# Kernel optimization log

Hardware: AMD Instinct MI355X
Metric: run time of the kernel (lower is better)

## Reference

```python
import jax, jax.numpy as jnp
import numpy as np

E = 16          # num_experts
D_FULL = 1024   # full_feature_dim
DM = 128        # expert_dim
S = D_FULL // E # per-expert feature slice = 64
P = 2048        # num patches
B = 8
C = 256
W = 3           # local_window (neighbor experts)
DEPTH = 8       # cantor_depth
NEG = -1e9


def _cantor_coord(pos, max_len, depth):
    x = pos / max(1, max_len - 1)
    x = max(1e-6, min(x, 1.0 - 1e-6))
    val, factor = 0.0, 0.5
    for _ in range(depth):
        x *= 3.0
        d = int(x)
        x -= d
        if d == 2:
            val += factor
        factor *= 0.5
    return val


def _expert_routes():
    coords = np.array([_cantor_coord(i, E, DEPTH) for i in range(E)], dtype=np.float32)
    return np.stack([np.argsort(np.abs(coords - coords[i]), kind='stable')[:W] for i in range(E)]).astype(np.int32)


ROUTES = _expert_routes()  # [E, W] static routing table


def setup_inputs():
    key = jax.random.key(0)
    ks = jax.random.split(key, 8)
    h = S // 4
    lim = float(np.sqrt(6.0 / (S + DM)))  # xavier_uniform bound
    penta = jax.random.normal(ks[5], (E, 5, DM), jnp.float32) * 0.02
    penta = penta / jnp.linalg.norm(penta, axis=-1, keepdims=True)
    return {
        'tokens': jax.random.normal(ks[0], (B, P, D_FULL), jnp.float32),
        'fingerprints': jax.random.uniform(ks[1], (P,), jnp.float32),
        'alpha': jnp.ones((E,), jnp.float32),
        'gate_w1': jax.random.normal(ks[2], (E, S, h), jnp.float32) * 0.05,
        'gate_b1': jnp.zeros((E, h), jnp.float32),
        'gate_w2': jax.random.normal(ks[3], (E, h, 1), jnp.float32) * 0.05,
        'gate_b2': jnp.zeros((E, 1), jnp.float32),
        'q_w': jax.random.uniform(ks[4], (E, S, DM), jnp.float32, -lim, lim),
        'k_w': jax.random.uniform(ks[6], (E, S, DM), jnp.float32, -lim, lim),
        'v_w': jax.random.uniform(ks[7], (E, S, DM), jnp.float32, -lim, lim),
        'penta': penta,
        'fusion_w': jnp.ones((5,), jnp.float32) / 5.0,
        'temperature': jnp.float32(0.5),
    }


def _dispatch(fingerprints):
    # Fingerprint band masks, then fixed-capacity gather (static shapes for jit).
    masks = []
    for e in range(E):
        lo, hi = e / E, (e + 1) / E
        m = (fingerprints >= lo) & ((fingerprints <= hi) if e == E - 1 else (fingerprints < hi))
        masks.append(m)
    masks = jnp.stack(masks)                             # [E, P]
    order = jnp.argsort(jnp.where(masks, 0, 1), axis=1)  # stable: assigned patches first
    idx = order[:, :C]                                   # [E, C]
    valid = jnp.take_along_axis(masks, idx, axis=1)      # [E, C]
    return idx, valid


def _forward(tokens, fingerprints, alpha, gate_w1, gate_b1, gate_w2, gate_b2,
             q_w, k_w, v_w, penta, fusion_w, temperature):
    idx, valid = _dispatch(fingerprints)
    Kaff, Qaff, Vs = [], [], []
    for e in range(E):  # fixed structural loop over experts
        feats = tokens[:, idx[e], e * S:(e + 1) * S]                       # [B, C, S]
        g = jax.nn.sigmoid(jax.nn.gelu(feats @ gate_w1[e] + gate_b1[e]) @ gate_w2[e] + gate_b2[e])
        aw = jax.nn.sigmoid(alpha[e])
        feats = feats * (g * aw + (1.0 - aw))                              # gated features
        Q = feats @ q_w[e]
        K = feats @ k_w[e]
        V = feats @ v_w[e]                                                 # [B, C, DM]
        dirs = penta[e] / jnp.linalg.norm(penta[e], axis=-1, keepdims=True)  # [5, DM]
        Kaff.append(jnp.einsum('bcd,vd->vbc', K, dirs))
        Qaff.append(jnp.einsum('bcd,vd->vbc', Q, dirs))
        Vs.append(V)
    Kaff = jnp.stack(Kaff)   # [E, 5, B, C]
    Qaff = jnp.stack(Qaff)   # [E, 5, B, C]
    Vs = jnp.stack(Vs)       # [E, B, C, DM]
    wdir = jax.nn.softmax(fusion_w)
    vmask = valid.astype(jnp.float32)
    out = jnp.zeros((B, P, DM), jnp.float32)
    for e in range(E):
        nb = ROUTES[e]                                  # static [W]
        Knb, Vnb, vnb = Kaff[nb], Vs[nb], vmask[nb]     # [W,5,B,C], [W,B,C,DM], [W,C]
        scores = jnp.einsum('vbi,nvbj->vbinj', Qaff[e], Knb) / temperature
        scores = jnp.where(vnb[None, None, None, :, :] > 0, scores, NEG)
        attn = jax.nn.softmax(scores.reshape(5, B, C, W * C), axis=-1).reshape(5, B, C, W, C)
        att = jnp.einsum('vbinj,nbjd->vbid', attn, Vnb)  # per-direction attended values
        out_e = jnp.einsum('v,vbid->bid', wdir, att) * vmask[e][None, :, None]
        out = out.at[:, idx[e]].add(out_e)              # scatter back to patch positions
    return out


def reference(tokens, fingerprints, alpha, gate_w1, gate_b1, gate_w2, gate_b2,
              q_w, k_w, v_w, penta, fusion_w, temperature):
    return _forward(tokens, fingerprints, alpha, gate_w1, gate_b1, gate_w2, gate_b2,
                    q_w, k_w, v_w, penta, fusion_w, temperature)
```

## Files before the change

kernel.cpp:

```cpp
#include <hip/hip_runtime.h>
#include <cfloat>
#include <math.h>

#define E 16
#define DFULL 1024
#define DM 128
#define S 64
#define P 2048
#define B 8
#define C 256
#define W 3
#define H 16
#define RQ 16
#define NCH 16
#define RQ2 32
#define NCH2 8
#define LOG2E 1.4426950408889634f
#define WST 272

typedef __attribute__((ext_vector_type(8))) short short8;
typedef __attribute__((ext_vector_type(4))) float f32x4;
#define MFMA_BF16(a, b, c) __builtin_amdgcn_mfma_f32_16x16x32_bf16((a), (b), (c), 0, 0, 0)

#if defined(__HIP_DEVICE_COMPILE__) && __has_builtin(__builtin_amdgcn_exp2f)
#define EXP2(x) __builtin_amdgcn_exp2f(x)
#else
#define EXP2(x) exp2f(x)
#endif

struct RoutesArg { int nb[E][W]; };

static void compute_routes(int r[E][W]) {
  float coords[E];
  for (int i = 0; i < E; ++i) {
    double x = (double)i / (double)(E - 1);
    if (x < 1e-06) x = 1e-06;
    if (x > 1.0 - 1e-06) x = 1.0 - 1e-06;
    double val = 0.0, factor = 0.5;
    for (int k = 0; k < 8; ++k) {
      x *= 3.0;
      int d = (int)x;
      x -= (double)d;
      if (d == 2) val += factor;
      factor *= 0.5;
    }
    coords[i] = (float)val;
  }
  for (int e = 0; e < E; ++e) {
    float de[E];
    for (int i = 0; i < E; ++i) de[i] = fabsf(coords[i] - coords[e]);
    bool used[E] = {false};
    for (int w = 0; w < W; ++w) {
      int best = -1; float bd = FLT_MAX;
      for (int i = 0; i < E; ++i)
        if (!used[i] && de[i] < bd) { bd = de[i]; best = i; }
      used[best] = true;
      r[e][w] = best;
    }
  }
}

__device__ __forceinline__ unsigned short bfhi(float x) {
  return (unsigned short)(__float_as_uint(x) >> 16);
}
__device__ __forceinline__ float bf2f(unsigned short h) {
  return __uint_as_float(((unsigned)h) << 16);
}
__device__ __forceinline__ float gelu_tanh(float x) {
  float u = 0.7978845608028654f * (x + 0.044715f * x * x * x);
  float ez = __expf(2.0f * u);
  float th = 1.0f - __fdividef(2.0f, ez + 1.0f);
  return 0.5f * x * (1.0f + th);
}
__device__ __forceinline__ float sigmoidf_(float x) {
  return __fdividef(1.0f, 1.0f + __expf(-x));
}

__global__ __launch_bounds__(256) void k_setup(
    const float* __restrict__ fp, const float* __restrict__ qw,
    const float* __restrict__ kw, const float* __restrict__ penta,
    const float* __restrict__ temp, const float* __restrict__ vw,
    int* __restrict__ idx, int* __restrict__ counts,
    unsigned short* __restrict__ qkdT_h, unsigned short* __restrict__ qkdT_l,
    unsigned short* __restrict__ vwT_h, unsigned short* __restrict__ vwT_l) {
  int e = blockIdx.x, t = threadIdx.x;
  __shared__ float s_tr[DM * 65];
  if (blockIdx.y == 1) {
    const float* vwe = vw + (size_t)e * S * DM;
    for (int u = t; u < S * DM; u += 256) {
      int s = u >> 7, d = u & 127;
      s_tr[d * 65 + s] = vwe[u];
    }
    __syncthreads();
    for (int u = t; u < S * DM; u += 256) {
      int d = u >> 6, s = u & 63;
      float f = s_tr[d * 65 + s];
      unsigned short h = bfhi(f), l = bfhi(f - bf2f(h));
      vwT_h[(size_t)e * 8192 + u] = h;
      vwT_l[(size_t)e * 8192 + u] = l;
    }
    return;
  }
  {
    float lo = (float)e * 0.0625f, hi = (float)(e + 1) * 0.0625f;
    bool last = (e == E - 1);
    int p0 = t * 8;
    int m[8]; int ls = 0;
    #pragma unroll
    for (int k = 0; k < 8; ++k) {
      float f = fp[p0 + k];
      bool mm = (f >= lo) && (last ? (f <= hi) : (f < hi));
      m[k] = mm ? 1 : 0;
      ls += m[k];
    }
    __shared__ int sc[256];
    sc[t] = ls;
    __syncthreads();
    for (int o = 1; o < 256; o <<= 1) {
      int v = (t >= o) ? sc[t - o] : 0;
      __syncthreads();
      sc[t] += v;
      __syncthreads();
    }
    int incl = sc[t];
    int M = sc[255];
    int r = incl - ls;
    #pragma unroll
    for (int k = 0; k < 8; ++k) {
      if (m[k]) {
        if (r < C) idx[e * C + r] = p0 + k;
        r++;
      }
    }
    if (t == 0) counts[e] = (M < C) ? M : C;
  }
  __syncthreads();
  __shared__ float s_rn[5];
  if (t < 5) {
    const float* pv = penta + (e * 5 + t) * DM;
    float ss = 0.f;
    for (int d = 0; d < DM; ++d) ss += pv[d] * pv[d];
    s_rn[t] = 1.0f / sqrtf(ss);
  }
  __syncthreads();
  float invT = 1.0f / temp[0];
  int s = t & 63, cg = t >> 6;
  for (int c = cg; c < 10; c += 4) {
    int v = c % 5;
    bool isq = (c < 5);
    const float* wrow = (isq ? qw : kw) + ((size_t)e * S + s) * DM;
    const float* pv = penta + (e * 5 + v) * DM;
    float acc = 0.f;
    #pragma unroll
    for (int d4 = 0; d4 < DM / 4; ++d4) {
      float4 a = ((const float4*)wrow)[d4];
      float4 p = ((const float4*)pv)[d4];
      acc += a.x * p.x + a.y * p.y + a.z * p.z + a.w * p.w;
    }
    float val = acc * s_rn[v] * (isq ? invT : 1.0f);
    unsigned short h = bfhi(val), l = bfhi(val - bf2f(h));
    qkdT_h[(e * 16 + c) * 64 + s] = h;
    qkdT_l[(e * 16 + c) * 64 + s] = l;
  }
  for (int c = 10 + cg; c < 16; c += 4) {
    qkdT_h[(e * 16 + c) * 64 + s] = 0;
    qkdT_l[(e * 16 + c) * 64 + s] = 0;
  }
}

__global__ __launch_bounds__(512, 8) void k_p1(
    const float* __restrict__ tokens, const float* __restrict__ alpha,
    const float* __restrict__ gw1, const float* __restrict__ gb1,
    const float* __restrict__ gw2, const float* __restrict__ gb2,
    const unsigned short* __restrict__ qkdT_h, const unsigned short* __restrict__ qkdT_l,
    const unsigned short* __restrict__ vwT_h, const unsigned short* __restrict__ vwT_l,
    const int* __restrict__ idx, const int* __restrict__ counts,
    float* __restrict__ Qa, float* __restrict__ Ka,
    unsigned short* __restrict__ Vt_h, unsigned short* __restrict__ Vt_l,
    float* __restrict__ kmx, float* __restrict__ kmn,
    float* __restrict__ out) {
  int e = blockIdx.x, b = blockIdx.y, rq = blockIdx.z;
  int t = threadIdx.x;

  {
    int blk = (e * B + b) * NCH + rq;
    if (t < 256) {
      float4 z4 = {0.f, 0.f, 0.f, 0.f};
      ((float4*)out)[(size_t)blk * 256 + t] = z4;
    }
  }

  int Me = counts[e];
  int r0 = rq * RQ;
  if (r0 >= Me) {
    if (t < 5) {
      kmx[((e * 5 + t) * B + b) * NCH + rq] = -FLT_MAX;
      kmn[((e * 5 + t) * B + b) * NCH + rq] = FLT_MAX;
    }
    return;
  }

  __shared__ float s_f[RQ * 65];
  __shared__ __align__(16) unsigned short s_fh[RQ * 72];
  __shared__ __align__(16) unsigned short s_fl[RQ * 72];
  __shared__ float s_gw1[S * H];
  __shared__ float s_gh[RQ * 8 * 17];
  __shared__ float s_scl[RQ];
  __shared__ float s_kx[5 * RQ], s_kn[5 * RQ];
  __shared__ __align__(16) unsigned short s_vth[DM * 16];
  __shared__ __align__(16) unsigned short s_vtl[DM * 16];

  if (t < 256) {
    int row = t >> 4, q4 = t & 15;
    int ii = r0 + row;
    int pos = (ii < Me) ? idx[e * C + ii] : idx[e * C];
    const float* trow = tokens + ((size_t)b * P + pos) * DFULL + e * S;
    float4 v4 = ((const float4*)trow)[q4];
    s_f[row * 65 + q4 * 4 + 0] = v4.x;
    s_f[row * 65 + q4 * 4 + 1] = v4.y;
    s_f[row * 65 + q4 * 4 + 2] = v4.z;
    s_f[row * 65 + q4 * 4 + 3] = v4.w;
    ((float4*)s_gw1)[t] = ((const float4*)(gw1 + (size_t)e * S * H))[t];
  }
  __syncthreads();

  if (t < 128) {
    int row = t >> 3, sq = t & 7;
    float hh[H];
    #pragma unroll
    for (int j = 0; j < H; ++j) hh[j] = 0.f;
    #pragma unroll
    for (int k = 0; k < 8; ++k) {
      int s = sq * 8 + k;
      float fs = s_f[row * 65 + s];
      const float* gr = s_gw1 + s * H;
      #pragma unroll
      for (int j = 0; j < H; ++j) hh[j] += fs * gr[j];
    }
    #pragma unroll
    for (int j = 0; j < H; ++j) s_gh[(row * 8 + sq) * 17 + j] = hh[j];
  }
  __syncthreads();
  if (t < 256) {
    int row = t >> 4, j = t & 15;
    float hj = gb1[e * H + j];
    #pragma unroll
    for (int p = 0; p < 8; ++p) hj += s_gh[(row * 8 + p) * 17 + j];
    float gz = gelu_tanh(hj) * gw2[e * H + j];
    #pragma unroll
    for (int off = 1; off < 16; off <<= 1) gz += __shfl_xor(gz, off);
    if (j == 0) {
      float aw = sigmoidf_(alpha[e]);
      s_scl[row] = sigmoidf_(gb2[e] + gz) * aw + (1.0f - aw);
    }
  }
  __syncthreads();
  if (t < 256) {
    int row = t >> 4, s0 = (t & 15) * 4;
    float sc = s_scl[row];
    #pragma unroll
    for (int k = 0; k < 4; ++k) {
      float f = s_f[row * 65 + s0 + k] * sc;
      unsigned short h = bfhi(f), l = bfhi(f - bf2f(h));
      s_fh[row * 72 + s0 + k] = h;
      s_fl[row * 72 + s0 + k] = l;
    }
  }
  __syncthreads();

  int L = t & 63, wv = t >> 6, quad = L >> 4, col = L & 15;

  {
    const unsigned short* vTh = vwT_h + (size_t)e * 8192;
    const unsigned short* vTl = vwT_l + (size_t)e * 8192;
    f32x4 va = {0.f, 0.f, 0.f, 0.f};
    int d0 = wv * 16 + col;
    #pragma unroll
    for (int kc = 0; kc < 2; ++kc) {
      int ko = kc * 32 + quad * 8;
      short8 ah = *(const short8*)(s_fh + col * 72 + ko);
      short8 al = *(const short8*)(s_fl + col * 72 + ko);
      short8 bh = *(const short8*)(vTh + d0 * 64 + ko);
      short8 bl = *(const short8*)(vTl + d0 * 64 + ko);
      va = MFMA_BF16(ah, bh, va);
      va = MFMA_BF16(ah, bl, va);
      va = MFMA_BF16(al, bh, va);
    }
    #pragma unroll
    for (int reg = 0; reg < 4; ++reg) {
      int row = quad * 4 + reg;
      float f0 = va[reg];
      unsigned short h0 = bfhi(f0), l0 = bfhi(f0 - bf2f(h0));
      s_vth[d0 * 16 + row] = h0;
      s_vtl[d0 * 16 + row] = l0;
    }
  }

  if (wv == 0) {
    const unsigned short* qTh = qkdT_h + e * 16 * 64;
    const unsigned short* qTl = qkdT_l + e * 16 * 64;
    f32x4 qa = {0.f, 0.f, 0.f, 0.f};
    #pragma unroll
    for (int kc = 0; kc < 2; ++kc) {
      int ko = kc * 32 + quad * 8;
      short8 ah = *(const short8*)(s_fh + col * 72 + ko);
      short8 al = *(const short8*)(s_fl + col * 72 + ko);
      short8 bh = *(const short8*)(qTh + col * 64 + ko);
      short8 bl = *(const short8*)(qTl + col * 64 + ko);
      qa = MFMA_BF16(ah, bh, qa);
      qa = MFMA_BF16(ah, bl, qa);
      qa = MFMA_BF16(al, bh, qa);
    }
    #pragma unroll
    for (int reg = 0; reg < 4; ++reg) {
      int row = quad * 4 + reg;
      int ii = r0 + row;
      float val = qa[reg];
      if (col < 5) {
        if (ii < Me) Qa[((e * 5 + col) * B + b) * C + ii] = val;
      } else if (col < 10) {
        int v = col - 5;
        if (ii < Me) Ka[((e * 5 + v) * B + b) * C + ii] = val;
        s_kx[v * RQ + row] = (ii < Me) ? val : -FLT_MAX;
        s_kn[v * RQ + row] = (ii < Me) ? val : FLT_MAX;
      }
    }
  }
  __syncthreads();
  if (t < 5) {
    float mx = -FLT_MAX, mn = FLT_MAX;
    for (int r = 0; r < RQ; ++r) {
      mx = fmaxf(mx, s_kx[t * RQ + r]);
      mn = fminf(mn, s_kn[t * RQ + r]);
    }
    kmx[((e * 5 + t) * B + b) * NCH + rq] = mx;
    kmn[((e * 5 + t) * B + b) * NCH + rq] = mn;
  }
  if (t < 256) {
    size_t base = (size_t)(e * B + b) * (DM * C);
    int jsl = t >> 7, d = t & 127;
    size_t dst = base + ((size_t)(rq * 2 + jsl) * DM + d) * 8;
    int src = d * 16 + jsl * 8;
    *(short8*)(Vt_h + dst) = *(const short8*)(s_vth + src);
    *(short8*)(Vt_l + dst) = *(const short8*)(s_vtl + src);
  }
}

__global__ __launch_bounds__(512, 6) void k_p2v(
    const float* __restrict__ Qa, const float* __restrict__ Ka,
    const unsigned short* __restrict__ Vt_h, const unsigned short* __restrict__ Vt_l,
    const float* __restrict__ kmx, const float* __restrict__ kmn,
    const int* __restrict__ idx, const int* __restrict__ counts,
    const float* __restrict__ fusw, float* __restrict__ out, RoutesArg R) {
  int e = blockIdx.x, b = blockIdx.y, rq = blockIdx.z;
  int t = threadIdx.x;
  int Me = counts[e];
  int r0 = rq * RQ2;
  if (r0 >= Me) return;

  __shared__ __align__(16) float s_ka[3 * 5 * C];
  __shared__ __align__(16) unsigned short s_wh[RQ2 * WST];
  __shared__ __align__(16) unsigned short s_wl[RQ2 * WST];
  __shared__ float s_l[5 * RQ2];
  __shared__ float s_KX[5], s_KN[5];
  float* s_lp = (float*)s_wh;

  int nbs[3] = {R.nb[e][0], R.nb[e][1], R.nb[e][2]};
  int Mns[3] = {counts[nbs[0]], counts[nbs[1]], counts[nbs[2]]};
  int row = t & 31, jq = t >> 5;
  int ii = r0 + row;
  int L = t & 63, wv = t >> 6, quad = L >> 4, col = L & 15;

  float qv[5];
  #pragma unroll
  for (int v = 0; v < 5; ++v)
    qv[v] = Qa[(((size_t)e * 5 + v) * B + b) * C + ii];
  float fw[5];
  #pragma unroll
  for (int v = 0; v < 5; ++v) fw[v] = fusw[v];

  for (int u = t; u < 960; u += 512) {
    int n = (u >= 640) ? 2 : ((u >= 320) ? 1 : 0);
    int r2 = u - n * 320;
    int v = r2 >> 6, off = r2 & 63;
    ((float4*)s_ka)[n * 320 + (v << 6) + off] =
        ((const float4*)(Ka + (((size_t)nbs[n] * 5 + v) * B + b) * C))[off];
  }
  if (wv < 5) {
    float KX = -FLT_MAX, KN = FLT_MAX;
    if (L < 48) {
      int n = L >> 4, k = L & 15;
      int base = ((nbs[n] * 5 + wv) * B + b) * NCH + k;
      KX = kmx[base];
      KN = kmn[base];
    }
    #pragma unroll
    for (int off = 32; off; off >>= 1) {
      KX = fmaxf(KX, __shfl_xor(KX, off));
      KN = fminf(KN, __shfl_xor(KN, off));
    }
    if (L == 0) { s_KX[wv] = KX; s_KN[wv] = KN; }
  }
  __syncthreads();

  float q2[5], m2[5];
  #pragma unroll
  for (int v = 0; v < 5; ++v) {
    q2[v] = qv[v] * LOG2E;
    m2[v] = ((qv[v] > 0.f) ? qv[v] * s_KX[v] : qv[v] * s_KN[v]) * LOG2E;
  }

  float lp[5] = {0.f, 0.f, 0.f, 0.f, 0.f};
  for (int n = 0; n < 3; ++n) {
    const float* ka_n = s_ka + n * 1280;
    int Mn = Mns[n];
    for (int j = jq; j < Mn; j += 16) {
      #pragma unroll
      for (int v = 0; v < 5; ++v)
        lp[v] += EXP2(fmaf(q2[v], ka_n[v * C + j], -m2[v]));
    }
  }
  #pragma unroll
  for (int v = 0; v < 5; ++v) lp[v] += __shfl_xor(lp[v], 32);
  if (L < 32) {
    #pragma unroll
    for (int v = 0; v < 5; ++v) s_lp[(wv * 5 + v) * RQ2 + L] = lp[v];
  }
  __syncthreads();
  if (t < 160) {
    int v = t >> 5, rw = t & 31;
    float l = 0.f;
    #pragma unroll
    for (int w = 0; w < 8; ++w) l += s_lp[(w * 5 + v) * RQ2 + rw];
    s_l[v * RQ2 + rw] = l;
  }
  __syncthreads();

  float fmx = fw[0];
  #pragma unroll
  for (int v = 1; v < 5; ++v) fmx = fmaxf(fmx, fw[v]);
  float fsum = 0.f;
  #pragma unroll
  for (int v = 0; v < 5; ++v) { fw[v] = __expf(fw[v] - fmx); fsum += fw[v]; }
  float rfs = __fdividef(1.0f, fsum);
  float c2[5];
  #pragma unroll
  for (int v = 0; v < 5; ++v) {
    float cl = __fdividef(fw[v] * rfs, s_l[v * RQ2 + row]);
    c2[v] = __log2f(cl) - m2[v];
  }

  int d0 = wv * 16 + col;
  f32x4 acc0 = {0.f, 0.f, 0.f, 0.f};
  f32x4 acc1 = {0.f, 0.f, 0.f, 0.f};

  for (int n = 0; n < 3; ++n) {
    int ne = nbs[n], Mn = Mns[n];
    int kcN = (Mn + 31) >> 5;
    const float* ka_n = s_ka + n * 1280;
    __syncthreads();
    const unsigned short* vbh = Vt_h + (size_t)(ne * B + b) * (DM * C);
    const unsigned short* vbl = Vt_l + (size_t)(ne * B + b) * (DM * C);
    size_t sb0 = ((size_t)quad * DM + d0) * 8;
    short8 bh = *(const short8*)(vbh + sb0);
    short8 bl = *(const short8*)(vbl + sb0);
    int jlim = kcN * 32;
    for (int j0 = jq * 8; j0 < jlim; j0 += 128) {
      short8 h8, l8;
      #pragma unroll
      for (int k2 = 0; k2 < 8; ++k2) {
        int jj = j0 + k2;
        float ww = 0.f;
        if (jj < Mn) {
          #pragma unroll
          for (int v = 0; v < 5; ++v)
            ww += EXP2(fmaf(q2[v], ka_n[v * C + jj], c2[v]));
        }
        unsigned short h = bfhi(ww), l = bfhi(ww - bf2f(h));
        h8[k2] = (short)h;
        l8[k2] = (short)l;
      }
      *(short8*)(s_wh + row * WST + j0) = h8;
      *(short8*)(s_wl + row * WST + j0) = l8;
    }
    __syncthreads();
    __builtin_amdgcn_s_setprio(1);
    for (int kc = 0; kc < kcN; ++kc) {
      int kn = (kc + 1 < kcN) ? (kc + 1) : kc;
      size_t sb = ((size_t)(kn * 4 + quad) * DM + d0) * 8;
      short8 nbh = *(const short8*)(vbh + sb);
      short8 nbl = *(const short8*)(vbl + sb);
      int ko = kc * 32 + quad * 8;
      short8 ah0 = *(const short8*)(s_wh + col * WST + ko);
      short8 al0 = *(const short8*)(s_wl + col * WST + ko);
      short8 ah1 = *(const short8*)(s_wh + (16 + col) * WST + ko);
      short8 al1 = *(const short8*)(s_wl + (16 + col) * WST + ko);
      acc0 = MFMA_BF16(ah0, bh, acc0);
      acc1 = MFMA_BF16(ah1, bh, acc1);
      acc0 = MFMA_BF16(ah0, bl, acc0);
      acc1 = MFMA_BF16(ah1, bl, acc1);
      acc0 = MFMA_BF16(al0, bh, acc0);
      acc1 = MFMA_BF16(al1, bh, acc1);
      bh = nbh;
      bl = nbl;
    }
    __builtin_amdgcn_s_setprio(0);
  }

  #pragma unroll
  for (int mt = 0; mt < 2; ++mt) {
    f32x4 a = mt ? acc1 : acc0;
    #pragma unroll
    for (int reg = 0; reg < 4; ++reg) {
      int rr = mt * 16 + quad * 4 + reg;
      int iw = r0 + rr;
      if (iw < Me) {
        int pos = idx[e * C + iw];
        out[((size_t)b * P + pos) * DM + d0] = a[reg];
      }
    }
  }
}

extern "C" void kernel_launch(void* const* d_in, const int* in_sizes, int n_in,
                              void* d_out, int out_size, void* d_ws, size_t ws_size,
                              hipStream_t stream) {
  const float* tokens = (const float*)d_in[0];
  const float* fingerprints = (const float*)d_in[1];
  const float* alpha = (const float*)d_in[2];
  const float* gw1 = (const float*)d_in[3];
  const float* gb1 = (const float*)d_in[4];
  const float* gw2 = (const float*)d_in[5];
  const float* gb2 = (const float*)d_in[6];
  const float* qw = (const float*)d_in[7];
  const float* kw = (const float*)d_in[8];
  const float* vw = (const float*)d_in[9];
  const float* penta = (const float*)d_in[10];
  const float* fusw = (const float*)d_in[11];
  const float* temp = (const float*)d_in[12];
  float* out = (float*)d_out;

  float* ws = (float*)d_ws;
  float* Qa = ws;
  float* Ka = Qa + (size_t)E * 5 * B * C;
  float* kmx = Ka + (size_t)E * 5 * B * C;
  float* kmn = kmx + (size_t)E * 5 * B * NCH;
  unsigned short* qkdT_h = (unsigned short*)(kmn + (size_t)E * 5 * B * NCH);
  unsigned short* qkdT_l = qkdT_h + (size_t)E * 16 * 64;
  unsigned short* vwT_h = qkdT_l + (size_t)E * 16 * 64;
  unsigned short* vwT_l = vwT_h + (size_t)E * S * DM;
  unsigned short* Vt_h = vwT_l + (size_t)E * S * DM;
  unsigned short* Vt_l = Vt_h + (size_t)E * B * DM * C;
  int* idx = (int*)(Vt_l + (size_t)E * B * DM * C);
  int* counts = idx + (size_t)E * C;

  RoutesArg R;
  compute_routes(R.nb);

  k_setup<<<dim3(E, 2), dim3(256), 0, stream>>>(fingerprints, qw, kw, penta, temp, vw,
                                                idx, counts, qkdT_h, qkdT_l, vwT_h, vwT_l);
  k_p1<<<dim3(E, B, NCH), dim3(512), 0, stream>>>(tokens, alpha, gw1, gb1, gw2, gb2,
                                                  qkdT_h, qkdT_l, vwT_h, vwT_l,
                                                  idx, counts, Qa, Ka, Vt_h, Vt_l,
                                                  kmx, kmn, out);
  k_p2v<<<dim3(E, B, NCH2), dim3(512), 0, stream>>>(Qa, Ka, Vt_h, Vt_l, kmx, kmn,
                                                    idx, counts, fusw, out, R);
}
```

Measured before the change: 171.5 us.

## Double k_p1 row tile to 32, use all threads, vectorize LDS reads in p2v

k_p1 now handles 32 rows per block instead of 16, so all 512 threads load tokens, compute the gate directly without a partial-sum stage, and each wave runs two MFMA tiles that reuse the same weight fragments. The key min/max reduction now uses shuffles. Shared buffers are aliased to limit LDS growth, and the grid is flattened to 2D. In k_p2v, the Ka reads for the exp sums are vectorized to float4 loads with masking applied after the exp, which trades extra exp work past Mn for fewer LDS loads and less branching. The halved block count in k_p1 may reduce latency hiding.

```diff
diff --git a/kernel.cpp b/kernel.cpp
--- a/kernel.cpp
+++ b/kernel.cpp
@@ -11,14 +11,16 @@
 #define C 256
 #define W 3
 #define H 16
-#define RQ 16
-#define NCH 16
+#define RQ1 32
+#define NCH1 8
 #define RQ2 32
 #define NCH2 8
 #define LOG2E 1.4426950408889634f
 #define WST 272
+#define SFT 68
 
 typedef __attribute__((ext_vector_type(8))) short short8;
+typedef __attribute__((ext_vector_type(4))) short short4v;
 typedef __attribute__((ext_vector_type(4))) float f32x4;
 #define MFMA_BF16(a, b, c) __builtin_amdgcn_mfma_f32_16x16x32_bf16((a), (b), (c), 0, 0, 0)
 
@@ -179,73 +181,60 @@
     unsigned short* __restrict__ Vt_h, unsigned short* __restrict__ Vt_l,
     float* __restrict__ kmx, float* __restrict__ kmn,
     float* __restrict__ out) {
-  int e = blockIdx.x, b = blockIdx.y, rq = blockIdx.z;
+  int g = blockIdx.x, rq = blockIdx.y;
+  int e = g >> 3, b = g & 7;
   int t = threadIdx.x;
 
   {
-    int blk = (e * B + b) * NCH + rq;
-    if (t < 256) {
-      float4 z4 = {0.f, 0.f, 0.f, 0.f};
-      ((float4*)out)[(size_t)blk * 256 + t] = z4;
-    }
+    int blk = g * NCH1 + rq;
+    float4 z4 = {0.f, 0.f, 0.f, 0.f};
+    ((float4*)out)[(size_t)blk * 512 + t] = z4;
   }
 
   int Me = counts[e];
-  int r0 = rq * RQ;
+  int r0 = rq * RQ1;
   if (r0 >= Me) {
     if (t < 5) {
-      kmx[((e * 5 + t) * B + b) * NCH + rq] = -FLT_MAX;
-      kmn[((e * 5 + t) * B + b) * NCH + rq] = FLT_MAX;
+      kmx[((e * 5 + t) * B + b) * NCH1 + rq] = -FLT_MAX;
+      kmn[((e * 5 + t) * B + b) * NCH1 + rq] = FLT_MAX;
     }
     return;
   }
 
-  __shared__ float s_f[RQ * 65];
-  __shared__ __align__(16) unsigned short s_fh[RQ * 72];
-  __shared__ __align__(16) unsigned short s_fl[RQ * 72];
-  __shared__ float s_gw1[S * H];
-  __shared__ float s_gh[RQ * 8 * 17];
-  __shared__ float s_scl[RQ];
-  __shared__ float s_kx[5 * RQ], s_kn[5 * RQ];
-  __shared__ __align__(16) unsigned short s_vth[DM * 16];
-  __shared__ __align__(16) unsigned short s_vtl[DM * 16];
-
-  if (t < 256) {
+  __shared__ __align__(16) char smemA[RQ1 * SFT * 4];
+  __shared__ __align__(16) char smemB[2 * DM * 16 * 2];
+  __shared__ __align__(16) unsigned short s_fh[RQ1 * 72];
+  __shared__ __align__(16) unsigned short s_fl[RQ1 * 72];
+  __shared__ float s_scl[RQ1];
+  __shared__ float s_kx[5 * RQ1], s_kn[5 * RQ1];
+  float* s_f = (float*)smemA;
+  unsigned short* s_vth = (unsigned short*)smemA;
+  float* s_gw1 = (float*)smemB;
+  unsigned short* s_vtl = (unsigned short*)smemB;
+
+  {
     int row = t >> 4, q4 = t & 15;
     int ii = r0 + row;
     int pos = (ii < Me) ? idx[e * C + ii] : idx[e * C];
     const float* trow = tokens + ((size_t)b * P + pos) * DFULL + e * S;
     float4 v4 = ((const float4*)trow)[q4];
-    s_f[row * 65 + q4 * 4 + 0] = v4.x;
-    s_f[row * 65 + q4 * 4 + 1] = v4.y;
-    s_f[row * 65 + q4 * 4 + 2] = v4.z;
-    s_f[row * 65 + q4 * 4 + 3] = v4.w;
-    ((float4*)s_gw1)[t] = ((const float4*)(gw1 + (size_t)e * S * H))[t];
-  }
-  __syncthreads();
-
-  if (t < 128) {
-    int row = t >> 3, sq = t & 7;
-    float hh[H];
-    #pragma unroll
-    for (int j = 0; j < H; ++j) hh[j] = 0.f;
-    #pragma unroll
-    for (int k = 0; k < 8; ++k) {
-      int s = sq * 8 + k;
-      float fs = s_f[row * 65 + s];
-      const float* gr = s_gw1 + s * H;
-      #pragma unroll
-      for (int j = 0; j < H; ++j) hh[j] += fs * gr[j];
-    }
-    #pragma unroll
-    for (int j = 0; j < H; ++j) s_gh[(row * 8 + sq) * 17 + j] = hh[j];
-  }
-  __syncthreads();
-  if (t < 256) {
+    *(float4*)(s_f + row * SFT + q4 * 4) = v4;
+    if (t < 256)
+      ((float4*)s_gw1)[t] = ((const float4*)(gw1 + (size_t)e * S * H))[t];
+  }
+  __syncthreads();
+
+  {
     int row = t >> 4, j = t & 15;
     float hj = gb1[e * H + j];
     #pragma unroll
-    for (int p = 0; p < 8; ++p) hj += s_gh[(row * 8 + p) * 17 + j];
+    for (int s4 = 0; s4 < 16; ++s4) {
+      float4 f4 = *(const float4*)(s_f + row * SFT + s4 * 4);
+      hj = fmaf(f4.x, s_gw1[(s4 * 4 + 0) * H + j], hj);
+      hj = fmaf(f4.y, s_gw1[(s4 * 4 + 1) * H + j], hj);
+      hj = fmaf(f4.z, s_gw1[(s4 * 4 + 2) * H + j], hj);
+      hj = fmaf(f4.w, s_gw1[(s4 * 4 + 3) * H + j], hj);
+    }
     float gz = gelu_tanh(hj) * gw2[e * H + j];
     #pragma unroll
     for (int off = 1; off < 16; off <<= 1) gz += __shfl_xor(gz, off);
@@ -255,16 +244,21 @@
     }
   }
   __syncthreads();
-  if (t < 256) {
+
+  {
     int row = t >> 4, s0 = (t & 15) * 4;
     float sc = s_scl[row];
+    float4 f4 = *(const float4*)(s_f + row * SFT + s0);
+    float fv[4] = {f4.x * sc, f4.y * sc, f4.z * sc, f4.w * sc};
+    short4v h4, l4;
     #pragma unroll
     for (int k = 0; k < 4; ++k) {
-      float f = s_f[row * 65 + s0 + k] * sc;
-      unsigned short h = bfhi(f), l = bfhi(f - bf2f(h));
-      s_fh[row * 72 + s0 + k] = h;
-      s_fl[row * 72 + s0 + k] = l;
-    }
+      unsigned short h = bfhi(fv[k]), l = bfhi(fv[k] - bf2f(h));
+      h4[k] = (short)h;
+      l4[k] = (short)l;
+    }
+    *(short4v*)(s_fh + row * 72 + s0) = h4;
+    *(short4v*)(s_fl + row * 72 + s0) = l4;
   }
   __syncthreads();
 
@@ -273,38 +267,47 @@
   {
     const unsigned short* vTh = vwT_h + (size_t)e * 8192;
     const unsigned short* vTl = vwT_l + (size_t)e * 8192;
-    f32x4 va = {0.f, 0.f, 0.f, 0.f};
+    f32x4 va0 = {0.f, 0.f, 0.f, 0.f};
+    f32x4 va1 = {0.f, 0.f, 0.f, 0.f};
     int d0 = wv * 16 + col;
     #pragma unroll
     for (int kc = 0; kc < 2; ++kc) {
       int ko = kc * 32 + quad * 8;
-      short8 ah = *(const short8*)(s_fh + col * 72 + ko);
-      short8 al = *(const short8*)(s_fl + col * 72 + ko);
       short8 bh = *(const short8*)(vTh + d0 * 64 + ko);
       short8 bl = *(const short8*)(vTl + d0 * 64 + ko);
-      va = MFMA_BF16(ah, bh, va);
-      va = MFMA_BF16(ah, bl, va);
-      va = MFMA_BF16(al, bh, va);
+      short8 ah0 = *(const short8*)(s_fh + col * 72 + ko);
+      short8 al0 = *(const short8*)(s_fl + col * 72 + ko);
+      short8 ah1 = *(const short8*)(s_fh + (16 + col) * 72 + ko);
+      short8 al1 = *(const short8*)(s_fl + (16 + col) * 72 + ko);
+      va0 = MFMA_BF16(ah0, bh, va0);
+      va1 = MFMA_BF16(ah1, bh, va1);
+      va0 = MFMA_BF16(ah0, bl, va0);
+      va1 = MFMA_BF16(ah1, bl, va1);
+      va0 = MFMA_BF16(al0, bh, va0);
+      va1 = MFMA_BF16(al1, bh, va1);
     }
     #pragma unroll
     for (int reg = 0; reg < 4; ++reg) {
       int row = quad * 4 + reg;
-      float f0 = va[reg];
+      float f0 = va0[reg], f1 = va1[reg];
       unsigned short h0 = bfhi(f0), l0 = bfhi(f0 - bf2f(h0));
+      unsigned short h1 = bfhi(f1), l1 = bfhi(f1 - bf2f(h1));
       s_vth[d0 * 16 + row] = h0;
       s_vtl[d0 * 16 + row] = l0;
-    }
-  }
-
-  if (wv == 0) {
+      s_vth[2048 + d0 * 16 + row] = h1;
+      s_vtl[2048 + d0 * 16 + row] = l1;
+    }
+  }
+
+  if (wv < 2) {
     const unsigned short* qTh = qkdT_h + e * 16 * 64;
     const unsigned short* qTl = qkdT_l + e * 16 * 64;
     f32x4 qa = {0.f, 0.f, 0.f, 0.f};
     #pragma unroll
     for (int kc = 0; kc < 2; ++kc) {
       int ko = kc * 32 + quad * 8;
-      short8 ah = *(const short8*)(s_fh + col * 72 + ko);
-      short8 al = *(const short8*)(s_fl + col * 72 + ko);
+      short8 ah = *(const short8*)(s_fh + (wv * 16 + col) * 72 + ko);
+      short8 al = *(const short8*)(s_fl + (wv * 16 + col) * 72 + ko);
       short8 bh = *(const short8*)(qTh + col * 64 + ko);
       short8 bl = *(const short8*)(qTl + col * 64 + ko);
       qa = MFMA_BF16(ah, bh, qa);
@@ -313,34 +316,40 @@
     }
     #pragma unroll
     for (int reg = 0; reg < 4; ++reg) {
-      int row = quad * 4 + reg;
-      int ii = r0 + row;
+      int rowl = wv * 16 + quad * 4 + reg;
+      int ii = r0 + rowl;
       float val = qa[reg];
       if (col < 5) {
         if (ii < Me) Qa[((e * 5 + col) * B + b) * C + ii] = val;
       } else if (col < 10) {
         int v = col - 5;
         if (ii < Me) Ka[((e * 5 + v) * B + b) * C + ii] = val;
-        s_kx[v * RQ + row] = (ii < Me) ? val : -FLT_MAX;
-        s_kn[v * RQ + row] = (ii < Me) ? val : FLT_MAX;
+        s_kx[v * RQ1 + rowl] = (ii < Me) ? val : -FLT_MAX;
+        s_kn[v * RQ1 + rowl] = (ii < Me) ? val : FLT_MAX;
       }
     }
   }
   __syncthreads();
-  if (t < 5) {
-    float mx = -FLT_MAX, mn = FLT_MAX;
-    for (int r = 0; r < RQ; ++r) {
-      mx = fmaxf(mx, s_kx[t * RQ + r]);
-      mn = fminf(mn, s_kn[t * RQ + r]);
-    }
-    kmx[((e * 5 + t) * B + b) * NCH + rq] = mx;
-    kmn[((e * 5 + t) * B + b) * NCH + rq] = mn;
-  }
-  if (t < 256) {
+
+  if (t < 160) {
+    int v = t >> 5, rw = t & 31;
+    float mx = s_kx[v * RQ1 + rw], mn = s_kn[v * RQ1 + rw];
+    #pragma unroll
+    for (int off = 16; off; off >>= 1) {
+      mx = fmaxf(mx, __shfl_xor(mx, off));
+      mn = fminf(mn, __shfl_xor(mn, off));
+    }
+    if (rw == 0) {
+      kmx[((e * 5 + v) * B + b) * NCH1 + rq] = mx;
+      kmn[((e * 5 + v) * B + b) * NCH1 + rq] = mn;
+    }
+  }
+  {
     size_t base = (size_t)(e * B + b) * (DM * C);
     int jsl = t >> 7, d = t & 127;
-    size_t dst = base + ((size_t)(rq * 2 + jsl) * DM + d) * 8;
-    int src = d * 16 + jsl * 8;
+    int tile = jsl >> 1, half = jsl & 1;
+    size_t dst = base + ((size_t)(rq * 4 + jsl) * DM + d) * 8;
+    int src = tile * 2048 + d * 16 + half * 8;
     *(short8*)(Vt_h + dst) = *(const short8*)(s_vth + src);
     *(short8*)(Vt_l + dst) = *(const short8*)(s_vtl + src);
   }
@@ -352,7 +361,8 @@
     const float* __restrict__ kmx, const float* __restrict__ kmn,
     const int* __restrict__ idx, const int* __restrict__ counts,
     const float* __restrict__ fusw, float* __restrict__ out, RoutesArg R) {
-  int e = blockIdx.x, b = blockIdx.y, rq = blockIdx.z;
+  int g = blockIdx.x, rq = blockIdx.y;
+  int e = g >> 3, b = g & 7;
   int t = threadIdx.x;
   int Me = counts[e];
   int r0 = rq * RQ2;
@@ -388,9 +398,9 @@
   }
   if (wv < 5) {
     float KX = -FLT_MAX, KN = FLT_MAX;
-    if (L < 48) {
-      int n = L >> 4, k = L & 15;
-      int base = ((nbs[n] * 5 + wv) * B + b) * NCH + k;
+    if (L < 24) {
+      int n = L >> 3, k = L & 7;
+      int base = ((nbs[n] * 5 + wv) * B + b) * NCH1 + k;
       KX = kmx[base];
       KN = kmn[base];
     }
@@ -414,10 +424,16 @@
   for (int n = 0; n < 3; ++n) {
     const float* ka_n = s_ka + n * 1280;
     int Mn = Mns[n];
-    for (int j = jq; j < Mn; j += 16) {
+    for (int jb = jq * 4; jb < Mn; jb += 64) {
       #pragma unroll
-      for (int v = 0; v < 5; ++v)
-        lp[v] += EXP2(fmaf(q2[v], ka_n[v * C + j], -m2[v]));
+      for (int v = 0; v < 5; ++v) {
+        f32x4 k4 = *(const f32x4*)(ka_n + v * C + jb);
+        #pragma unroll
+        for (int u = 0; u < 4; ++u) {
+          float ex = EXP2(fmaf(q2[v], k4[u], -m2[v]));
+          lp[v] += ((jb + u) < Mn) ? ex : 0.f;
+        }
+      }
     }
   }
   #pragma unroll
@@ -466,16 +482,23 @@
     short8 bl = *(const short8*)(vbl + sb0);
     int jlim = kcN * 32;
     for (int j0 = jq * 8; j0 < jlim; j0 += 128) {
+      f32x4 kaA[5], kaB[5];
+      #pragma unroll
+      for (int v = 0; v < 5; ++v) {
+        kaA[v] = *(const f32x4*)(ka_n + v * C + j0);
+        kaB[v] = *(const f32x4*)(ka_n + v * C + j0 + 4);
+      }
       short8 h8, l8;
       #pragma unroll
       for (int k2 = 0; k2 < 8; ++k2) {
         int jj = j0 + k2;
-        float ww = 0.f;
-        if (jj < Mn) {
-          #pragma unroll
-          for (int v = 0; v < 5; ++v)
-            ww += EXP2(fmaf(q2[v], ka_n[v * C + jj], c2[v]));
+        float s5 = 0.f;
+        #pragma unroll
+        for (int v = 0; v < 5; ++v) {
+          float kv = (k2 < 4) ? kaA[v][k2] : kaB[v][k2 - 4];
+          s5 += EXP2(fmaf(q2[v], kv, c2[v]));
         }
+        float ww = (jj < Mn) ? s5 : 0.f;
         unsigned short h = bfhi(ww), l = bfhi(ww - bf2f(h));
         h8[k2] = (short)h;
         l8[k2] = (short)l;
@@ -544,8 +567,8 @@
   float* Qa = ws;
   float* Ka = Qa + (size_t)E * 5 * B * C;
   float* kmx = Ka + (size_t)E * 5 * B * C;
-  float* kmn = kmx + (size_t)E * 5 * B * NCH;
-  unsigned short* qkdT_h = (unsigned short*)(kmn + (size_t)E * 5 * B * NCH);
+  float* kmn = kmx + (size_t)E * 5 * B * 16;
+  unsigned short* qkdT_h = (unsigned short*)(kmn + (size_t)E * 5 * B * 16);
   unsigned short* qkdT_l = qkdT_h + (size_t)E * 16 * 64;
   unsigned short* vwT_h = qkdT_l + (size_t)E * 16 * 64;
   unsigned short* vwT_l = vwT_h + (size_t)E * S * DM;
@@ -559,10 +582,10 @@
 
   k_setup<<<dim3(E, 2), dim3(256), 0, stream>>>(fingerprints, qw, kw, penta, temp, vw,
                                                 idx, counts, qkdT_h, qkdT_l, vwT_h, vwT_l);
-  k_p1<<<dim3(E, B, NCH), dim3(512), 0, stream>>>(tokens, alpha, gw1, gb1, gw2, gb2,
-                                                  qkdT_h, qkdT_l, vwT_h, vwT_l,
-                                                  idx, counts, Qa, Ka, Vt_h, Vt_l,
-                                                  kmx, kmn, out);
-  k_p2v<<<dim3(E, B, NCH2), dim3(512), 0, stream>>>(Qa, Ka, Vt_h, Vt_l, kmx, kmn,
-                                                    idx, counts, fusw, out, R);
-}
+  k_p1<<<dim3(E * B, NCH1), dim3(512), 0, stream>>>(tokens, alpha, gw1, gb1, gw2, gb2,
+                                                    qkdT_h, qkdT_l, vwT_h, vwT_l,
+                                                    idx, counts, Qa, Ka, Vt_h, Vt_l,
+                                                    kmx, kmn, out);
+  k_p2v<<<dim3(E * B, NCH2), dim3(512), 0, stream>>>(Qa, Ka, Vt_h, Vt_l, kmx, kmn,
+                                                     idx, counts, fusw, out, R);
+}
```

Result: slower. 177.2 us (+3.3%).
